# Optimization experiments

Hardware: AMD Instinct MI355X
Metric: run time of the kernel (lower is better)

Reference implementation:

```python
import jax, jax.numpy as jnp
import numpy as np

N = 30000        # nodes
E = 480000       # edges
IN_DIM = 128
HID = 64
OUT = 64
POS_DIM = 32
H = 4            # heads (same for all layers)
PVOCAB = 3
NEG_SLOPE = 0.2


def _xavier(key, shape):
    fan_in, fan_out = shape[0], shape[-1] if len(shape) > 1 else shape[0]
    scale = 1.414 * np.sqrt(2.0 / (fan_in + fan_out))
    return jax.random.normal(key, shape, dtype=jnp.float32) * scale


def setup_inputs() -> dict:
    key = jax.random.key(0)
    ks = jax.random.split(key, 20)
    d0_in = IN_DIM + POS_DIM            # 160
    d_mid = HID * H + POS_DIM           # 288
    inp = {
        "features": jax.random.normal(ks[0], (N, IN_DIM), dtype=jnp.float32),
        # layer 0
        "W0": _xavier(ks[1], (d0_in, H * HID)),
        "al0": _xavier(ks[2], (H, HID)),
        "ar0": _xavier(ks[3], (H, HID)),
        "pe0": _xavier(ks[4], (PVOCAB, POS_DIM)),
        # layer 1
        "W1": _xavier(ks[5], (d_mid, H * HID)),
        "al1": _xavier(ks[6], (H, HID)),
        "ar1": _xavier(ks[7], (H, HID)),
        "pe1": _xavier(ks[8], (PVOCAB, POS_DIM)),
        # output layer
        "W2": _xavier(ks[9], (d_mid, H * OUT)),
        "al2": _xavier(ks[10], (H, OUT)),
        "ar2": _xavier(ks[11], (H, OUT)),
        "pe2": _xavier(ks[12], (PVOCAB, POS_DIM)),
        # graph
        "src": jax.random.randint(ks[13], (E,), 0, N, dtype=jnp.int32),
        "dst": jax.random.randint(ks[14], (E,), 0, N, dtype=jnp.int32),
        "pos": jax.random.randint(ks[15], (N,), 0, PVOCAB, dtype=jnp.int32),
    }
    return inp


def gat_layer(h, W, a_l, a_r, src, dst):
    # h: [N, in_d]; W: [in_d, H*d]; a_l,a_r: [H, d]
    n = h.shape[0]
    nh, d = a_l.shape
    ft = (h @ W).reshape(n, nh, d)                       # [N,H,d]
    a1 = jnp.einsum("nhd,hd->nh", ft, a_l)               # [N,H]
    a2 = jnp.einsum("nhd,hd->nh", ft, a_r)               # [N,H]
    e = jax.nn.leaky_relu(a1[src] + a2[dst], NEG_SLOPE)  # [E,H]
    # per-destination segment softmax (numerically stable)
    m = jax.ops.segment_max(e, dst, num_segments=n)      # [N,H]
    ex = jnp.exp(e - m[dst])                             # [E,H]
    s = jax.ops.segment_sum(ex, dst, num_segments=n)     # [N,H]
    alpha = ex / s[dst]                                  # [E,H]
    msg = ft[src] * alpha[:, :, None]                    # [E,H,d]
    return jax.ops.segment_sum(msg, dst, num_segments=n) # [N,H,d]


def reference(features, W0, al0, ar0, pe0, W1, al1, ar1, pe1,
              W2, al2, ar2, pe2, src, dst, pos):
    h = features
    # hidden GAT layers with ELU activation and head-flattening
    for W, al, ar, pe in ((W0, al0, ar0, pe0), (W1, al1, ar1, pe1)):
        p = pe[pos]                                      # [N, pos_dim]
        hcat = jnp.concatenate((h, p), axis=1)
        out = gat_layer(hcat, W, al, ar, src, dst)       # [N,H,d]
        h = jax.nn.elu(out.reshape(out.shape[0], -1))    # [N,H*d]
    # output layer: mean over heads
    p = pe2[pos]
    hcat = jnp.concatenate((h, p), axis=1)
    out = gat_layer(hcat, W2, al2, ar2, src, dst)        # [N,H,out]
    return out.mean(axis=1)                              # [N,out]
```

## Files before the change

### kernel.cpp

```cpp
#include <hip/hip_runtime.h>
#include <hip/hip_fp16.h>
#include <math.h>

#define N_NODES 30000
#define N_EDGES 480000
#define HEADS 4
#define DHEAD 64
#define FDIM 256
#define POSD 32
#define CAPB 96
#define HIST_NB 1875

typedef _Float16 half8 __attribute__((ext_vector_type(8)));
typedef float floatx4 __attribute__((ext_vector_type(4)));

__device__ __forceinline__ float lrelu(float x){ return x > 0.f ? x : 0.2f * x; }

__global__ __launch_bounds__(256) void bucketprep_k(
    const int* __restrict__ src, const int* __restrict__ dst,
    int* __restrict__ deg, int* __restrict__ esrc,
    const float* __restrict__ W0, const float* __restrict__ W1,
    const float* __restrict__ W2, _Float16* __restrict__ T0,
    _Float16* __restrict__ T1, _Float16* __restrict__ T2,
    const float* __restrict__ pe0, const float* __restrict__ pe1,
    const float* __restrict__ pe2, float* __restrict__ PW){
  int blk = blockIdx.x;
  if (blk < HIST_NB){
    int e = blk * 256 + threadIdx.x;
    if (e < N_EDGES){
      int d = dst[e];
      int slot = atomicAdd(&deg[d], 1);
      if (slot < CAPB) esrc[d * CAPB + slot] = src[e];
    }
  } else if (blk < HIST_NB + 192){
    int q = blk - HIST_NB;
    int l = q >> 6, kk0 = q & 63;
    const float* W = l == 0 ? W0 : (l == 1 ? W1 : W2);
    _Float16* T    = l == 0 ? T0 : (l == 1 ? T1 : T2);
    int K = l == 0 ? 128 : 256;
    int n = threadIdx.x;
    for (int k = kk0; k < K; k += 64)
      T[(size_t)n * K + k] = (_Float16)W[(size_t)k * FDIM + n];
  } else {
    int q = blk - HIST_NB - 192;
    int layer = q / 3, v = q % 3;
    const float* W  = layer == 0 ? W0 : (layer == 1 ? W1 : W2);
    const float* pe = layer == 0 ? pe0 : (layer == 1 ? pe1 : pe2);
    int K = layer == 0 ? 128 : 256;
    int j = threadIdx.x;
    float s = 0.f;
#pragma unroll
    for (int k = 0; k < POSD; k++)
      s = fmaf(pe[v * POSD + k], W[(size_t)(K + k) * FDIM + j], s);
    PW[(layer * 3 + v) * FDIM + j] = s;
  }
}

template<typename T>
__global__ __launch_bounds__(256, 1) void gemm_mfma_k(
    const T* __restrict__ A, const _Float16* __restrict__ Wt,
    const float* __restrict__ PW, const int* __restrict__ pos,
    const float* __restrict__ al, const float* __restrict__ arw,
    _Float16* __restrict__ Ch, float* __restrict__ a1, float* __restrict__ a2,
    int K){
  int t = threadIdx.x;
  int w = t >> 6;
  int lane = t & 63;
  int lm = lane & 15;
  int kq = lane >> 4;
  int h0 = blockIdx.x * 2;
  int rowBase = blockIdx.y * 256 + w * 64;
  int colBase = h0 * 64;

  floatx4 acc[4][8] = {};

  const T* Ar[4];
#pragma unroll
  for (int r = 0; r < 4; r++)
    Ar[r] = A + (size_t)min(rowBase + r * 16 + lm, N_NODES - 1) * K;
  const _Float16* Bp[8];
#pragma unroll
  for (int j = 0; j < 8; j++)
    Bp[j] = Wt + (size_t)(colBase + j * 16 + lm) * K;

  for (int kb = 0; kb < K; kb += 32){
    int ko = kb + kq * 8;
    half8 bf[8];
#pragma unroll
    for (int j = 0; j < 8; j++) bf[j] = *(const half8*)(Bp[j] + ko);
#pragma unroll
    for (int r = 0; r < 4; r++){
      half8 af;
      if constexpr (sizeof(T) == 2){
        af = *(const half8*)(Ar[r] + ko);
      } else {
        float4 u0 = *(const float4*)(Ar[r] + ko);
        float4 u1 = *(const float4*)(Ar[r] + ko + 4);
        af[0] = (_Float16)u0.x; af[1] = (_Float16)u0.y;
        af[2] = (_Float16)u0.z; af[3] = (_Float16)u0.w;
        af[4] = (_Float16)u1.x; af[5] = (_Float16)u1.y;
        af[6] = (_Float16)u1.z; af[7] = (_Float16)u1.w;
      }
#pragma unroll
      for (int j = 0; j < 8; j++)
        acc[r][j] = __builtin_amdgcn_mfma_f32_16x16x32_f16(af, bf[j], acc[r][j], 0, 0, 0);
    }
  }

  float alw[8], arr[8];
#pragma unroll
  for (int j = 0; j < 8; j++){
    int hh = h0 + (j >> 2);
    int col = (j & 3) * 16 + lm;
    alw[j] = al [hh * DHEAD + col];
    arr[j] = arw[hh * DHEAD + col];
  }

#pragma unroll
  for (int r = 0; r < 4; r++){
#pragma unroll
    for (int p = 0; p < 4; p++){
      int row = rowBase + r * 16 + kq * 4 + p;
      if (row >= N_NODES) continue;
      int pz = pos[row];
      const float* pwb = PW + pz * FDIM + colBase;
      float s1a = 0.f, s2a = 0.f, s1b = 0.f, s2b = 0.f;
#pragma unroll
      for (int j = 0; j < 8; j++){
        float v = acc[r][j][p] + pwb[j * 16 + lm];
        Ch[(size_t)row * FDIM + colBase + j * 16 + lm] = (_Float16)v;
        if (j < 4){ s1a = fmaf(v, alw[j], s1a); s2a = fmaf(v, arr[j], s2a); }
        else      { s1b = fmaf(v, alw[j], s1b); s2b = fmaf(v, arr[j], s2b); }
      }
#pragma unroll
      for (int o2 = 1; o2 <= 8; o2 <<= 1){
        s1a += __shfl_xor(s1a, o2, 64); s2a += __shfl_xor(s2a, o2, 64);
        s1b += __shfl_xor(s1b, o2, 64); s2b += __shfl_xor(s2b, o2, 64);
      }
      if (lm == 0){
        a1[row * HEADS + h0]     = s1a;
        a2[row * HEADS + h0]     = s2a;
        a1[row * HEADS + h0 + 1] = s1b;
        a2[row * HEADS + h0 + 1] = s2b;
      }
    }
  }
}

__global__ __launch_bounds__(256) void agg4_k(
    const _Float16* __restrict__ ft, const float* __restrict__ a1,
    const float* __restrict__ a2, const int* __restrict__ degv,
    const int* __restrict__ esrc, _Float16* __restrict__ outh,
    float* __restrict__ outf, int mode){
  int wv = threadIdx.x >> 6;
  int lane = threadIdx.x & 63;
  int n = blockIdx.x * 4 + wv;
  if (n >= N_NODES) return;
  int jb = n * CAPB;
  int deg = min(degv[n], CAPB);
  int eidx = lane & 15, h = lane >> 4;
  int hsel = h << 4;
  float a2n = a2[n * HEADS + h];
  float4 acc = make_float4(0.f, 0.f, 0.f, 0.f);
  const _Float16* ftl = ft + lane * 4;
  struct h4 { __half2 a, b; };

  if (deg <= 64){
    int sreg[4]; float wreg[4];
    float m = -INFINITY;
#pragma unroll
    for (int r = 0; r < 4; r++){
      int idx = eidx + r * 16;
      int s = (idx < deg) ? esrc[jb + idx] : 0;
      sreg[r] = s;
      float e = (idx < deg) ? lrelu(a1[s * HEADS + h] + a2n) : -INFINITY;
      wreg[r] = e;
      m = fmaxf(m, e);
    }
    m = fmaxf(m, __shfl_xor(m, 1, 64));
    m = fmaxf(m, __shfl_xor(m, 2, 64));
    m = fmaxf(m, __shfl_xor(m, 4, 64));
    m = fmaxf(m, __shfl_xor(m, 8, 64));
    float ss = 0.f;
#pragma unroll
    for (int r = 0; r < 4; r++){
      int idx = eidx + r * 16;
      float tv = (idx < deg) ? __expf(wreg[r] - m) : 0.f;
      wreg[r] = tv;
      ss += tv;
    }
    ss += __shfl_xor(ss, 1, 64);
    ss += __shfl_xor(ss, 2, 64);
    ss += __shfl_xor(ss, 4, 64);
    ss += __shfl_xor(ss, 8, 64);
    float inv = (ss > 0.f) ? 1.f / ss : 0.f;
#pragma unroll
    for (int r = 0; r < 4; r++) wreg[r] *= inv;

#pragma unroll
    for (int r = 0; r < 4; r++){
      if (r * 16 >= deg) break;
      int lim = deg - r * 16; if (lim > 16) lim = 16;
      float wr = wreg[r]; int sr = sreg[r];
      int jj = 0;
      for (; jj + 8 <= lim; jj += 8){
        float w8[8]; int s8[8]; h4 f8[8];
#pragma unroll
        for (int u = 0; u < 8; u++){
          w8[u] = __shfl(wr, (jj + u) | hsel, 64);
          s8[u] = __shfl(sr, jj + u, 64);
        }
#pragma unroll
        for (int u = 0; u < 8; u++)
          f8[u] = *(const h4*)(ftl + (size_t)s8[u] * FDIM);
#pragma unroll
        for (int u = 0; u < 8; u++){
          float2 fa = __half22float2(f8[u].a), fb = __half22float2(f8[u].b);
          acc.x = fmaf(w8[u], fa.x, acc.x);
          acc.y = fmaf(w8[u], fa.y, acc.y);
          acc.z = fmaf(w8[u], fb.x, acc.z);
          acc.w = fmaf(w8[u], fb.y, acc.w);
        }
      }
      for (; jj < lim; jj += 4){
        float w4[4]; int s4[4]; h4 f4[4];
#pragma unroll
        for (int u = 0; u < 4; u++){
          w4[u] = __shfl(wr, (jj + u) | hsel, 64);
          s4[u] = __shfl(sr, jj + u, 64);
        }
#pragma unroll
        for (int u = 0; u < 4; u++)
          f4[u] = *(const h4*)(ftl + (size_t)s4[u] * FDIM);
#pragma unroll
        for (int u = 0; u < 4; u++){
          float2 fa = __half22float2(f4[u].a), fb = __half22float2(f4[u].b);
          acc.x = fmaf(w4[u], fa.x, acc.x);
          acc.y = fmaf(w4[u], fa.y, acc.y);
          acc.z = fmaf(w4[u], fb.x, acc.z);
          acc.w = fmaf(w4[u], fb.y, acc.w);
        }
      }
    }
  } else {
    float m = -INFINITY;
    for (int idx = eidx; idx < deg; idx += 16){
      int s = esrc[jb + idx];
      m = fmaxf(m, lrelu(a1[s * HEADS + h] + a2n));
    }
    m = fmaxf(m, __shfl_xor(m, 1, 64));
    m = fmaxf(m, __shfl_xor(m, 2, 64));
    m = fmaxf(m, __shfl_xor(m, 4, 64));
    m = fmaxf(m, __shfl_xor(m, 8, 64));
    float ss = 0.f;
    for (int idx = eidx; idx < deg; idx += 16){
      int s = esrc[jb + idx];
      ss += __expf(lrelu(a1[s * HEADS + h] + a2n) - m);
    }
    ss += __shfl_xor(ss, 1, 64);
    ss += __shfl_xor(ss, 2, 64);
    ss += __shfl_xor(ss, 4, 64);
    ss += __shfl_xor(ss, 8, 64);
    float inv = (ss > 0.f) ? 1.f / ss : 0.f;
    for (int j = 0; j < deg; j++){
      int sj = esrc[jb + j];
      float e = lrelu(a1[sj * HEADS + h] + a2n);
      float wj = __expf(e - m) * inv;
      h4 f = *(const h4*)(ftl + (size_t)sj * FDIM);
      float2 fa = __half22float2(f.a), fb = __half22float2(f.b);
      acc.x = fmaf(wj, fa.x, acc.x);
      acc.y = fmaf(wj, fa.y, acc.y);
      acc.z = fmaf(wj, fb.x, acc.z);
      acc.w = fmaf(wj, fb.y, acc.w);
    }
  }

  if (mode == 0){
    acc.x = acc.x > 0.f ? acc.x : (__expf(acc.x) - 1.f);
    acc.y = acc.y > 0.f ? acc.y : (__expf(acc.y) - 1.f);
    acc.z = acc.z > 0.f ? acc.z : (__expf(acc.z) - 1.f);
    acc.w = acc.w > 0.f ? acc.w : (__expf(acc.w) - 1.f);
    struct h4s { _Float16 h[4]; } u;
    u.h[0] = (_Float16)acc.x; u.h[1] = (_Float16)acc.y;
    u.h[2] = (_Float16)acc.z; u.h[3] = (_Float16)acc.w;
    *(h4s*)&outh[(size_t)n * FDIM + lane * 4] = u;
  } else {
#pragma unroll
    for (int o2 = 16; o2 <= 32; o2 <<= 1){
      acc.x += __shfl_xor(acc.x, o2, 64);
      acc.y += __shfl_xor(acc.y, o2, 64);
      acc.z += __shfl_xor(acc.z, o2, 64);
      acc.w += __shfl_xor(acc.w, o2, 64);
    }
    if (lane < 16){
      float4 o;
      o.x = acc.x * 0.25f; o.y = acc.y * 0.25f;
      o.z = acc.z * 0.25f; o.w = acc.w * 0.25f;
      *(float4*)&outf[(size_t)n * DHEAD + lane * 4] = o;
    }
  }
}

extern "C" void kernel_launch(void* const* d_in, const int* in_sizes, int n_in,
                              void* d_out, int out_size, void* d_ws, size_t ws_size,
                              hipStream_t stream){
  const float* features = (const float*)d_in[0];
  const float* W0  = (const float*)d_in[1];
  const float* al0 = (const float*)d_in[2];
  const float* ar0 = (const float*)d_in[3];
  const float* pe0 = (const float*)d_in[4];
  const float* W1  = (const float*)d_in[5];
  const float* al1 = (const float*)d_in[6];
  const float* ar1 = (const float*)d_in[7];
  const float* pe1 = (const float*)d_in[8];
  const float* W2  = (const float*)d_in[9];
  const float* al2 = (const float*)d_in[10];
  const float* ar2 = (const float*)d_in[11];
  const float* pe2 = (const float*)d_in[12];
  const int* srcv  = (const int*)d_in[13];
  const int* dstv  = (const int*)d_in[14];
  const int* posv  = (const int*)d_in[15];
  float* out = (float*)d_out;

  char* wp = (char*)d_ws;
  auto alloc = [&](size_t bytes){
    void* p = (void*)wp;
    wp += (bytes + 255) & ~(size_t)255;
    return p;
  };
  _Float16* fth   = (_Float16*)alloc(sizeof(_Float16) * (size_t)N_NODES * FDIM);
  _Float16* hbuf  = (_Float16*)alloc(sizeof(_Float16) * (size_t)N_NODES * FDIM);
  _Float16* Wt0   = (_Float16*)alloc(sizeof(_Float16) * 256 * 128);
  _Float16* Wt1   = (_Float16*)alloc(sizeof(_Float16) * 256 * 256);
  _Float16* Wt2   = (_Float16*)alloc(sizeof(_Float16) * 256 * 256);
  float* a1     = (float*)alloc(sizeof(float) * N_NODES * HEADS);
  float* a2     = (float*)alloc(sizeof(float) * N_NODES * HEADS);
  float* PW     = (float*)alloc(sizeof(float) * 9 * FDIM);
  int*   deg    = (int*)alloc(sizeof(int) * N_NODES);
  int*   esrc   = (int*)alloc(sizeof(int) * (size_t)N_NODES * CAPB);

  hipMemsetAsync(deg, 0, sizeof(int) * N_NODES, stream);
  bucketprep_k<<<HIST_NB + 201, 256, 0, stream>>>(
      srcv, dstv, deg, esrc, W0, W1, W2, Wt0, Wt1, Wt2,
      pe0, pe1, pe2, PW);

  dim3 ggrid(2, (N_NODES + 255) / 256);
  int agrid = (N_NODES + 3) / 4;

  gemm_mfma_k<float><<<ggrid, 256, 0, stream>>>(
      features, Wt0, PW + 0 * 3 * FDIM, posv, al0, ar0, fth, a1, a2, 128);
  agg4_k<<<agrid, 256, 0, stream>>>(fth, a1, a2, deg, esrc, hbuf, nullptr, 0);

  gemm_mfma_k<_Float16><<<ggrid, 256, 0, stream>>>(
      hbuf, Wt1, PW + 1 * 3 * FDIM, posv, al1, ar1, fth, a1, a2, 256);
  agg4_k<<<agrid, 256, 0, stream>>>(fth, a1, a2, deg, esrc, hbuf, nullptr, 0);

  gemm_mfma_k<_Float16><<<ggrid, 256, 0, stream>>>(
      hbuf, Wt2, PW + 2 * 3 * FDIM, posv, al2, ar2, fth, a1, a2, 256);
  agg4_k<<<agrid, 256, 0, stream>>>(fth, a1, a2, deg, esrc, nullptr, out, 1);
}
```

Before: 292.0 us.

## Shrink GEMM tiles and fuse layer-0 GEMM with edge bucketing and weight prep

The GEMM tile per block shrinks from 256 rows by two heads to 128 rows by one head, with launch bounds allowing two blocks per CU, so the grid has more blocks and occupancy is higher. The layer-0 GEMM is merged into one launch with the edge bucketing, the W1/W2 transposes and the positional projections, so independent work runs concurrently. The memset is folded into a small prep kernel that handles W0 and PW0. In exchange, each A row tile is now reloaded for every head, and the fused blocks compete for CU resources.

```diff
diff --git a/kernel.cpp b/kernel.cpp
--- a/kernel.cpp
+++ b/kernel.cpp
@@ -10,55 +10,16 @@
 #define POSD 32
 #define CAPB 96
 #define HIST_NB 1875
+#define G0_NB 940
 
 typedef _Float16 half8 __attribute__((ext_vector_type(8)));
 typedef float floatx4 __attribute__((ext_vector_type(4)));
 
 __device__ __forceinline__ float lrelu(float x){ return x > 0.f ? x : 0.2f * x; }
 
-__global__ __launch_bounds__(256) void bucketprep_k(
-    const int* __restrict__ src, const int* __restrict__ dst,
-    int* __restrict__ deg, int* __restrict__ esrc,
-    const float* __restrict__ W0, const float* __restrict__ W1,
-    const float* __restrict__ W2, _Float16* __restrict__ T0,
-    _Float16* __restrict__ T1, _Float16* __restrict__ T2,
-    const float* __restrict__ pe0, const float* __restrict__ pe1,
-    const float* __restrict__ pe2, float* __restrict__ PW){
-  int blk = blockIdx.x;
-  if (blk < HIST_NB){
-    int e = blk * 256 + threadIdx.x;
-    if (e < N_EDGES){
-      int d = dst[e];
-      int slot = atomicAdd(&deg[d], 1);
-      if (slot < CAPB) esrc[d * CAPB + slot] = src[e];
-    }
-  } else if (blk < HIST_NB + 192){
-    int q = blk - HIST_NB;
-    int l = q >> 6, kk0 = q & 63;
-    const float* W = l == 0 ? W0 : (l == 1 ? W1 : W2);
-    _Float16* T    = l == 0 ? T0 : (l == 1 ? T1 : T2);
-    int K = l == 0 ? 128 : 256;
-    int n = threadIdx.x;
-    for (int k = kk0; k < K; k += 64)
-      T[(size_t)n * K + k] = (_Float16)W[(size_t)k * FDIM + n];
-  } else {
-    int q = blk - HIST_NB - 192;
-    int layer = q / 3, v = q % 3;
-    const float* W  = layer == 0 ? W0 : (layer == 1 ? W1 : W2);
-    const float* pe = layer == 0 ? pe0 : (layer == 1 ? pe1 : pe2);
-    int K = layer == 0 ? 128 : 256;
-    int j = threadIdx.x;
-    float s = 0.f;
-#pragma unroll
-    for (int k = 0; k < POSD; k++)
-      s = fmaf(pe[v * POSD + k], W[(size_t)(K + k) * FDIM + j], s);
-    PW[(layer * 3 + v) * FDIM + j] = s;
-  }
-}
-
 template<typename T>
-__global__ __launch_bounds__(256, 1) void gemm_mfma_k(
-    const T* __restrict__ A, const _Float16* __restrict__ Wt,
+__device__ __forceinline__ void gemm_body(
+    int bx, int by, const T* __restrict__ A, const _Float16* __restrict__ Wt,
     const float* __restrict__ PW, const int* __restrict__ pos,
     const float* __restrict__ al, const float* __restrict__ arw,
     _Float16* __restrict__ Ch, float* __restrict__ a1, float* __restrict__ a2,
@@ -68,28 +29,28 @@
   int lane = t & 63;
   int lm = lane & 15;
   int kq = lane >> 4;
-  int h0 = blockIdx.x * 2;
-  int rowBase = blockIdx.y * 256 + w * 64;
-  int colBase = h0 * 64;
-
-  floatx4 acc[4][8] = {};
-
-  const T* Ar[4];
-#pragma unroll
-  for (int r = 0; r < 4; r++)
+  int h = bx;
+  int rowBase = by * 128 + w * 32;
+  int colBase = h * DHEAD;
+
+  floatx4 acc[2][4] = {};
+
+  const T* Ar[2];
+#pragma unroll
+  for (int r = 0; r < 2; r++)
     Ar[r] = A + (size_t)min(rowBase + r * 16 + lm, N_NODES - 1) * K;
-  const _Float16* Bp[8];
-#pragma unroll
-  for (int j = 0; j < 8; j++)
+  const _Float16* Bp[4];
+#pragma unroll
+  for (int j = 0; j < 4; j++)
     Bp[j] = Wt + (size_t)(colBase + j * 16 + lm) * K;
 
   for (int kb = 0; kb < K; kb += 32){
     int ko = kb + kq * 8;
-    half8 bf[8];
-#pragma unroll
-    for (int j = 0; j < 8; j++) bf[j] = *(const half8*)(Bp[j] + ko);
-#pragma unroll
-    for (int r = 0; r < 4; r++){
+    half8 bf[4];
+#pragma unroll
+    for (int j = 0; j < 4; j++) bf[j] = *(const half8*)(Bp[j] + ko);
+#pragma unroll
+    for (int r = 0; r < 2; r++){
       half8 af;
       if constexpr (sizeof(T) == 2){
         af = *(const half8*)(Ar[r] + ko);
@@ -102,48 +63,121 @@
         af[6] = (_Float16)u1.z; af[7] = (_Float16)u1.w;
       }
 #pragma unroll
-      for (int j = 0; j < 8; j++)
+      for (int j = 0; j < 4; j++)
         acc[r][j] = __builtin_amdgcn_mfma_f32_16x16x32_f16(af, bf[j], acc[r][j], 0, 0, 0);
     }
   }
 
-  float alw[8], arr[8];
-#pragma unroll
-  for (int j = 0; j < 8; j++){
-    int hh = h0 + (j >> 2);
-    int col = (j & 3) * 16 + lm;
-    alw[j] = al [hh * DHEAD + col];
-    arr[j] = arw[hh * DHEAD + col];
-  }
-
-#pragma unroll
-  for (int r = 0; r < 4; r++){
+  float alw[4], arr[4];
+#pragma unroll
+  for (int j = 0; j < 4; j++){
+    int col = j * 16 + lm;
+    alw[j] = al [h * DHEAD + col];
+    arr[j] = arw[h * DHEAD + col];
+  }
+
+#pragma unroll
+  for (int r = 0; r < 2; r++){
 #pragma unroll
     for (int p = 0; p < 4; p++){
       int row = rowBase + r * 16 + kq * 4 + p;
       if (row >= N_NODES) continue;
       int pz = pos[row];
       const float* pwb = PW + pz * FDIM + colBase;
-      float s1a = 0.f, s2a = 0.f, s1b = 0.f, s2b = 0.f;
-#pragma unroll
-      for (int j = 0; j < 8; j++){
+      float s1 = 0.f, s2 = 0.f;
+#pragma unroll
+      for (int j = 0; j < 4; j++){
         float v = acc[r][j][p] + pwb[j * 16 + lm];
         Ch[(size_t)row * FDIM + colBase + j * 16 + lm] = (_Float16)v;
-        if (j < 4){ s1a = fmaf(v, alw[j], s1a); s2a = fmaf(v, arr[j], s2a); }
-        else      { s1b = fmaf(v, alw[j], s1b); s2b = fmaf(v, arr[j], s2b); }
+        s1 = fmaf(v, alw[j], s1);
+        s2 = fmaf(v, arr[j], s2);
       }
 #pragma unroll
       for (int o2 = 1; o2 <= 8; o2 <<= 1){
-        s1a += __shfl_xor(s1a, o2, 64); s2a += __shfl_xor(s2a, o2, 64);
-        s1b += __shfl_xor(s1b, o2, 64); s2b += __shfl_xor(s2b, o2, 64);
+        s1 += __shfl_xor(s1, o2, 64);
+        s2 += __shfl_xor(s2, o2, 64);
       }
       if (lm == 0){
-        a1[row * HEADS + h0]     = s1a;
-        a2[row * HEADS + h0]     = s2a;
-        a1[row * HEADS + h0 + 1] = s1b;
-        a2[row * HEADS + h0 + 1] = s2b;
-      }
-    }
+        a1[row * HEADS + h] = s1;
+        a2[row * HEADS + h] = s2;
+      }
+    }
+  }
+}
+
+template<typename T>
+__global__ __launch_bounds__(256, 2) void gemm_k(
+    const T* __restrict__ A, const _Float16* __restrict__ Wt,
+    const float* __restrict__ PW, const int* __restrict__ pos,
+    const float* __restrict__ al, const float* __restrict__ arw,
+    _Float16* __restrict__ Ch, float* __restrict__ a1, float* __restrict__ a2,
+    int K){
+  gemm_body<T>(blockIdx.x, blockIdx.y, A, Wt, PW, pos, al, arw, Ch, a1, a2, K);
+}
+
+__global__ __launch_bounds__(256) void prep0_k(
+    const float* __restrict__ W0, const float* __restrict__ pe0,
+    _Float16* __restrict__ T0, float* __restrict__ PW,
+    int* __restrict__ deg){
+  int blk = blockIdx.x;
+  int n = threadIdx.x;
+  if (blk < 64){
+    for (int k = blk; k < 128; k += 64)
+      T0[(size_t)n * 128 + k] = (_Float16)W0[(size_t)k * FDIM + n];
+  } else if (blk < 67){
+    int v = blk - 64;
+    float s = 0.f;
+#pragma unroll
+    for (int k = 0; k < POSD; k++)
+      s = fmaf(pe0[v * POSD + k], W0[(size_t)(128 + k) * FDIM + n], s);
+    PW[v * FDIM + n] = s;
+  } else {
+    int i = (blk - 67) * 256 + n;
+    if (i < N_NODES) deg[i] = 0;
+  }
+}
+
+__global__ __launch_bounds__(256, 2) void fused0_k(
+    const float* __restrict__ A, const _Float16* __restrict__ Wt0,
+    const float* __restrict__ PW0, const int* __restrict__ pos,
+    const float* __restrict__ al0, const float* __restrict__ ar0,
+    _Float16* __restrict__ Ch, float* __restrict__ a1, float* __restrict__ a2,
+    const int* __restrict__ src, const int* __restrict__ dst,
+    int* __restrict__ deg, int* __restrict__ esrc,
+    const float* __restrict__ W1, const float* __restrict__ W2,
+    _Float16* __restrict__ T1, _Float16* __restrict__ T2,
+    const float* __restrict__ pe1, const float* __restrict__ pe2,
+    float* __restrict__ PWall){
+  int blk = blockIdx.x;
+  if (blk < G0_NB){
+    gemm_body<float>(blk & 3, blk >> 2, A, Wt0, PW0, pos, al0, ar0,
+                     Ch, a1, a2, 128);
+  } else if (blk < G0_NB + HIST_NB){
+    int e = (blk - G0_NB) * 256 + threadIdx.x;
+    if (e < N_EDGES){
+      int d = dst[e];
+      int slot = atomicAdd(&deg[d], 1);
+      if (slot < CAPB) esrc[d * CAPB + slot] = src[e];
+    }
+  } else if (blk < G0_NB + HIST_NB + 128){
+    int q = blk - G0_NB - HIST_NB;
+    int l = q >> 6, kk0 = q & 63;
+    const float* W = l == 0 ? W1 : W2;
+    _Float16* T    = l == 0 ? T1 : T2;
+    int n = threadIdx.x;
+    for (int k = kk0; k < 256; k += 64)
+      T[(size_t)n * 256 + k] = (_Float16)W[(size_t)k * FDIM + n];
+  } else {
+    int q = blk - G0_NB - HIST_NB - 128;
+    int layer = q / 3 + 1, v = q % 3;
+    const float* W  = layer == 1 ? W1 : W2;
+    const float* pe = layer == 1 ? pe1 : pe2;
+    int j = threadIdx.x;
+    float s = 0.f;
+#pragma unroll
+    for (int k = 0; k < POSD; k++)
+      s = fmaf(pe[v * POSD + k], W[(size_t)(256 + k) * FDIM + j], s);
+    PWall[(layer * 3 + v) * FDIM + j] = s;
   }
 }
 
@@ -339,23 +373,22 @@
   int*   deg    = (int*)alloc(sizeof(int) * N_NODES);
   int*   esrc   = (int*)alloc(sizeof(int) * (size_t)N_NODES * CAPB);
 
-  hipMemsetAsync(deg, 0, sizeof(int) * N_NODES, stream);
-  bucketprep_k<<<HIST_NB + 201, 256, 0, stream>>>(
-      srcv, dstv, deg, esrc, W0, W1, W2, Wt0, Wt1, Wt2,
-      pe0, pe1, pe2, PW);
-
-  dim3 ggrid(2, (N_NODES + 255) / 256);
+  prep0_k<<<185, 256, 0, stream>>>(W0, pe0, Wt0, PW, deg);
+
+  fused0_k<<<G0_NB + HIST_NB + 134, 256, 0, stream>>>(
+      features, Wt0, PW, posv, al0, ar0, fth, a1, a2,
+      srcv, dstv, deg, esrc, W1, W2, Wt1, Wt2, pe1, pe2, PW);
+
+  dim3 ggrid(4, (N_NODES + 127) / 128);
   int agrid = (N_NODES + 3) / 4;
 
-  gemm_mfma_k<float><<<ggrid, 256, 0, stream>>>(
-      features, Wt0, PW + 0 * 3 * FDIM, posv, al0, ar0, fth, a1, a2, 128);
   agg4_k<<<agrid, 256, 0, stream>>>(fth, a1, a2, deg, esrc, hbuf, nullptr, 0);
 
-  gemm_mfma_k<_Float16><<<ggrid, 256, 0, stream>>>(
+  gemm_k<_Float16><<<ggrid, 256, 0, stream>>>(
       hbuf, Wt1, PW + 1 * 3 * FDIM, posv, al1, ar1, fth, a1, a2, 256);
   agg4_k<<<agrid, 256, 0, stream>>>(fth, a1, a2, deg, esrc, hbuf, nullptr, 0);
 
-  gemm_mfma_k<_Float16><<<ggrid, 256, 0, stream>>>(
+  gemm_k<_Float16><<<ggrid, 256, 0, stream>>>(
       hbuf, Wt2, PW + 2 * 3 * FDIM, posv, al2, ar2, fth, a1, a2, 256);
   agg4_k<<<agrid, 256, 0, stream>>>(fth, a1, a2, deg, esrc, nullptr, out, 1);
 }
```

New measurement: 289.0 us. No clear change (-1.0%).
